# Optimization experiments

Hardware: AMD Instinct MI355X
Metric: run time of the kernel (lower is better)

The kernel has to match this reference:

```python
import jax, jax.numpy as jnp
import numpy as np

# Batched-graph geometry: 128 graphs x 400 nodes x 6400 edges
N_GRAPHS = 128
NODES_PER = 400
EDGES_PER = 6400
N_NODES = N_GRAPHS * NODES_PER      # 51200
N_EDGES = N_GRAPHS * EDGES_PER      # 819200
F_IN = 256
HID = 64
K = 8          # num_filtrations
D = 3          # outputs per coordinate function (4 funs -> 12 total)


def coord_feats(p, t_tri, t_gau, sig, W_lin, b_lin, c_rh, r_rh):
    """Apply the 4 coordinate transforms to persistence pairs p: [K, M, 2].
    Returns [M, K*4D] with layout cat-over-coordfuns inside, cat-over-filtrations outside,
    matching torch: cat([cat([mod(p_k) for mod in funs],1) for k],1)."""
    x0, x1 = p[..., 0:1], p[..., 1:2]                       # [K,M,1]
    tri = jax.nn.relu(x1 - jnp.abs(t_tri - x0))             # Triangle_transform -> [K,M,D]
    d2 = jnp.sum((p[..., None, :] - t_gau) ** 2, axis=-1)   # [K,M,D]
    gau = jnp.exp(-d2 / (2.0 * sig[0] ** 2))                # Gaussian_transform
    lin = p @ W_lin + b_lin                                 # Line_transform
    l1 = jnp.abs(x0 - c_rh) + jnp.abs(x1 - c_rh)            # L1 dist to centers
    rh = 1.0 / (1.0 + l1) - 1.0 / (1.0 + jnp.abs(jnp.abs(r_rh[0]) - l1))  # RationalHat
    feats = jnp.concatenate([tri, gau, lin, rh], axis=-1)   # [K,M,4D]
    Kk, M, Dd = feats.shape
    return feats.transpose(1, 0, 2).reshape(M, Kk * Dd)     # [M, K*4D]


def setup_inputs() -> dict:
    key = jax.random.key(0)
    ks = jax.random.split(key, 24)
    x = jax.random.normal(ks[0], (N_NODES, F_IN), jnp.float32)
    # edges drawn within each graph block
    offs = (jnp.arange(N_EDGES) // EDGES_PER) * NODES_PER
    edge_index = jax.random.randint(ks[1], (2, N_EDGES), 0, NODES_PER) + offs[None, :]
    batch_vec = jnp.arange(N_NODES) // NODES_PER            # graph id per node
    edge_slices = jnp.arange(N_GRAPHS + 1) * EDGES_PER
    s = lambda i, shape: (jax.random.normal(ks[i], shape, jnp.float32) * 0.1)
    inp = dict(
        x=x, edge_index=edge_index, batch_vec=batch_vec, edge_slices=edge_slices,
        # shared filtration MLP: Linear(F_IN,HID)-ReLU-Linear(HID,K)-ReLU
        W1=s(2, (F_IN, HID)), b1=jnp.zeros((HID,), jnp.float32),
        W2=s(3, (HID, K)), b2=jnp.zeros((K,), jnp.float32),
        # dim-0 coordinate-function params
        t_tri0=s(4, (D,)), t_gau0=s(5, (D, 2)), sig0=jnp.ones((1,), jnp.float32),
        W_lin0=s(6, (2, D)), b_lin0=jnp.zeros((D,), jnp.float32),
        c_rh0=s(7, (D,)), r_rh0=jnp.ones((1,), jnp.float32),
        # dim-1 coordinate-function params
        t_tri1=s(8, (D,)), t_gau1=s(9, (D, 2)), sig1=jnp.ones((1,), jnp.float32),
        W_lin1=s(10, (2, D)), b_lin1=jnp.zeros((D,), jnp.float32),
        c_rh1=s(11, (D,)), r_rh1=jnp.ones((1,), jnp.float32),
        # output linear: in = F_IN + 2*K*4D (dist_dim1=True, non-residual path)
        W_out=s(12, (F_IN + 2 * K * 4 * D, F_IN)), b_out=jnp.zeros((F_IN,), jnp.float32),
    )
    return inp


def reference(x, edge_index, batch_vec, edge_slices,
              W1, b1, W2, b2,
              t_tri0, t_gau0, sig0, W_lin0, b_lin0, c_rh0, r_rh0,
              t_tri1, t_gau1, sig1, W_lin1, b_lin1, c_rh1, r_rh1,
              W_out, b_out):
    # per-node filtration values (shared params, relu_filtrations)
    fv = jax.nn.relu(jax.nn.relu(x @ W1 + b1) @ W2 + b2)            # [N,K]
    # edge filtration = max of endpoint values
    fe = jnp.maximum(fv[edge_index[0]], fv[edge_index[1]])          # [E,K]
    # fake dim-0 persistence: pairs (v, v) for every vertex, per filtration
    pers0 = jnp.broadcast_to(fv.T[..., None], (K, fv.shape[0], 2))  # [K,N,2]
    # fake dim-1: one unpaired tuple per graph = max edge value, placed at first edge
    eb = batch_vec[edge_index[0]]                                   # [E] graph id per edge
    unpaired = jax.ops.segment_max(fe, eb, num_segments=N_GRAPHS)   # [B,K]
    chosen = edge_slices[:-1]                                       # deterministic edge per graph
    pers1 = jnp.zeros((edge_index.shape[1], K, 2), fv.dtype)
    pers1 = pers1.at[chosen, :, 0].set(unpaired)
    pers1 = pers1.transpose(1, 0, 2)                                # [K,E,2]
    # coordinate-function activations
    act0 = coord_feats(pers0, t_tri0, t_gau0, sig0, W_lin0, b_lin0, c_rh0, r_rh0)  # [N, K*12]
    mask = jnp.any(pers1 != 0, axis=(0, 2))                         # [E]
    act1 = coord_feats(pers1, t_tri1, t_gau1, sig1, W_lin1, b_lin1, c_rh1, r_rh1)  # [E, K*12]
    g1 = jax.ops.segment_sum(act1 * mask[:, None].astype(act1.dtype), eb,
                             num_segments=N_GRAPHS)                 # [B, K*12]
    concat = jnp.concatenate([x, act0, g1[batch_vec]], axis=1)      # [N, F_IN + 2*K*12]
    return jax.nn.relu(concat @ W_out + b_out)                      # [N, F_IN]
```

## Files before the change

kernel.cpp:

```cpp
#include <hip/hip_runtime.h>

#define N_GRAPHS 128
#define NODES_PER 400
#define EDGES_PER 6400
#define N_NODES (N_GRAPHS * NODES_PER)
#define N_EDGES (N_GRAPHS * EDGES_PER)
#define F_IN 256
#define HID 64
#define FEAT 96

typedef __attribute__((ext_vector_type(8))) short bf16x8;
typedef __attribute__((ext_vector_type(4))) float f32x4;

union u4b8 { uint4 u; bf16x8 v; };

__device__ __forceinline__ unsigned short f2b(float f) {
  union { float f; unsigned int u; } c; c.f = f;
  const unsigned int r = c.u + 0x7FFFu + ((c.u >> 16) & 1u);
  return (unsigned short)(r >> 16);
}

__device__ __forceinline__ void gload16(const void* g, void* l) {
  __builtin_amdgcn_global_load_lds(
      (const __attribute__((address_space(1))) unsigned int*)g,
      (__attribute__((address_space(3))) unsigned int*)l, 16, 0, 0);
}

__device__ __forceinline__ float coord_one(
    int fun, int d, float x0, float x1,
    const float* __restrict__ t_tri, const float* __restrict__ t_gau,
    const float* __restrict__ sig, const float* __restrict__ W_lin,
    const float* __restrict__ b_lin, const float* __restrict__ c_rh,
    const float* __restrict__ r_rh) {
  if (fun == 0) {
    return fmaxf(x1 - fabsf(t_tri[d] - x0), 0.f);
  } else if (fun == 1) {
    const float dx = x0 - t_gau[d * 2 + 0];
    const float dy = x1 - t_gau[d * 2 + 1];
    const float s = sig[0];
    return expf(-(dx * dx + dy * dy) / (2.f * s * s));
  } else if (fun == 2) {
    return x0 * W_lin[d] + x1 * W_lin[3 + d] + b_lin[d];
  } else {
    const float l1 = fabsf(x0 - c_rh[d]) + fabsf(x1 - c_rh[d]);
    return 1.f / (1.f + l1) - 1.f / (1.f + fabsf(fabsf(r_rh[0]) - l1));
  }
}

__global__ __launch_bounds__(256) void k_wt(
    const float* __restrict__ W_out, const float* __restrict__ W1,
    unsigned short* __restrict__ Wt2, unsigned short* __restrict__ Wt1c) {
  const int idx = blockIdx.x * 256 + threadIdx.x;
  if (idx < 384 * 256) {
    const int k = idx >> 8, c = idx & 255;
    const float v = (k < 352) ? W_out[(size_t)k * 256 + c] : 0.f;
    Wt2[((size_t)(k >> 3) * 256 + c) * 8 + (k & 7)] = f2b(v);
  } else {
    const int j = idx - 384 * 256;
    const int k = j >> 6, c = j & 63;
    Wt1c[((size_t)(k >> 3) * 64 + c) * 8 + (k & 7)] = f2b(W1[j]);
  }
}

__global__ __launch_bounds__(256, 3) void k_fv(
    const float* __restrict__ x, const unsigned short* __restrict__ Wt1c,
    const float* __restrict__ b1, const float* __restrict__ W2,
    const float* __restrict__ b2,
    const float* __restrict__ t_tri, const float* __restrict__ t_gau,
    const float* __restrict__ sig, const float* __restrict__ W_lin,
    const float* __restrict__ b_lin, const float* __restrict__ c_rh,
    const float* __restrict__ r_rh,
    float* __restrict__ fv, unsigned short* __restrict__ ext,
    unsigned short* __restrict__ xb, const int write_xb) {
  __shared__ float W2s[HID * 8];
  __shared__ float Hs[4][16][68];
  const int tid = threadIdx.x;
  const int wave = tid >> 6, lane = tid & 63;
  const int l15 = lane & 15, l4 = lane >> 4;
  const int n0 = blockIdx.x * 64;

  W2s[tid] = W2[tid];
  W2s[tid + 256] = W2[tid + 256];
  __syncthreads();

  const int arow = n0 + wave * 16 + l15;
  bf16x8 afr[8];
  #pragma unroll
  for (int kt = 0; kt < 8; ++kt) {
    const size_t go = (size_t)arow * F_IN + kt * 32 + l4 * 8;
    const float4 f0 = *(const float4*)&x[go];
    const float4 f1 = *(const float4*)&x[go + 4];
    u4b8 w;
    w.u.x = (unsigned)f2b(f0.x) | ((unsigned)f2b(f0.y) << 16);
    w.u.y = (unsigned)f2b(f0.z) | ((unsigned)f2b(f0.w) << 16);
    w.u.z = (unsigned)f2b(f1.x) | ((unsigned)f2b(f1.y) << 16);
    w.u.w = (unsigned)f2b(f1.z) | ((unsigned)f2b(f1.w) << 16);
    if (write_xb) *(uint4*)&xb[go] = w.u;
    afr[kt] = w.v;
  }

  f32x4 acc[4];
  #pragma unroll
  for (int nf = 0; nf < 4; ++nf) acc[nf] = (f32x4){0.f, 0.f, 0.f, 0.f};
  #pragma unroll
  for (int kt = 0; kt < 8; ++kt) {
    const unsigned short* wb = Wt1c + (size_t)(kt * 4 + l4) * 512;
    #pragma unroll
    for (int nf = 0; nf < 4; ++nf) {
      const bf16x8 b = *(const bf16x8*)&wb[(nf * 16 + l15) * 8];
      acc[nf] = __builtin_amdgcn_mfma_f32_16x16x32_bf16(afr[kt], b, acc[nf], 0, 0, 0);
    }
  }

  #pragma unroll
  for (int nf = 0; nf < 4; ++nf) {
    const int col = nf * 16 + l15;
    const float bb = b1[col];
    #pragma unroll
    for (int j = 0; j < 4; ++j)
      Hs[wave][l4 * 4 + j][col] = fmaxf(acc[nf][j] + bb, 0.f);
  }
  __syncthreads();

  #pragma unroll
  for (int p = tid; p < 512; p += 256) {
    const int row = p >> 3, kk = p & 7;
    const float* hr = Hs[row >> 4][row & 15];
    float s = b2[kk];
    #pragma unroll 8
    for (int j = 0; j < HID; ++j) s = fmaf(hr[j], W2s[j * 8 + kk], s);
    s = fmaxf(s, 0.f);
    const int n = n0 + row;
    fv[(size_t)n * 8 + kk] = s;

    unsigned short o[12] __attribute__((aligned(16)));
    #pragma unroll
    for (int fun = 0; fun < 4; ++fun)
      #pragma unroll
      for (int d = 0; d < 3; ++d)
        o[fun * 3 + d] = f2b(coord_one(fun, d, s, s,
                             t_tri, t_gau, sig, W_lin, b_lin, c_rh, r_rh));
    unsigned short* dst = &ext[(size_t)n * FEAT + kk * 12];
    *(uint2*)&dst[0] = *(const uint2*)&o[0];
    *(uint2*)&dst[4] = *(const uint2*)&o[4];
    *(uint2*)&dst[8] = *(const uint2*)&o[8];
  }
}

#define CHUNK (EDGES_PER / 8)
__global__ __launch_bounds__(256) void k_unpaired(
    const int* __restrict__ ei, const float* __restrict__ fv,
    float* __restrict__ unp) {
  __shared__ float lfv[NODES_PER * 8];
  __shared__ float red[256][8];
  const int g = blockIdx.x >> 3, ch = blockIdx.x & 7;
  const int tid = threadIdx.x;

  for (int i = tid; i < NODES_PER * 2; i += 256)
    *(float4*)&lfv[i * 4] = *(const float4*)&fv[(size_t)g * NODES_PER * 8 + i * 4];
  __syncthreads();

  float lm[8];
  #pragma unroll
  for (int k = 0; k < 8; ++k) lm[k] = 0.f;
  const int e0 = g * EDGES_PER + ch * CHUNK;
  for (int e = e0 + tid; e < e0 + CHUNK; e += 256) {
    const int a = ei[e] - g * NODES_PER;
    const int b = ei[N_EDGES + e] - g * NODES_PER;
    const float4 a0 = *(const float4*)&lfv[a * 8];
    const float4 a1 = *(const float4*)&lfv[a * 8 + 4];
    const float4 b0 = *(const float4*)&lfv[b * 8];
    const float4 b1 = *(const float4*)&lfv[b * 8 + 4];
    lm[0] = fmaxf(lm[0], fmaxf(a0.x, b0.x));
    lm[1] = fmaxf(lm[1], fmaxf(a0.y, b0.y));
    lm[2] = fmaxf(lm[2], fmaxf(a0.z, b0.z));
    lm[3] = fmaxf(lm[3], fmaxf(a0.w, b0.w));
    lm[4] = fmaxf(lm[4], fmaxf(a1.x, b1.x));
    lm[5] = fmaxf(lm[5], fmaxf(a1.y, b1.y));
    lm[6] = fmaxf(lm[6], fmaxf(a1.z, b1.z));
    lm[7] = fmaxf(lm[7], fmaxf(a1.w, b1.w));
  }
  #pragma unroll
  for (int k = 0; k < 8; ++k) red[tid][k] = lm[k];
  __syncthreads();
  for (int s = 128; s > 0; s >>= 1) {
    if (tid < s) {
      #pragma unroll
      for (int k = 0; k < 8; ++k)
        red[tid][k] = fmaxf(red[tid][k], red[tid + s][k]);
    }
    __syncthreads();
  }
  if (tid < 8)
    atomicMax((int*)&unp[g * 8 + tid], __float_as_int(red[0][tid]));
}

__global__ __launch_bounds__(256) void k_g1G(
    const float* __restrict__ unp, const float* __restrict__ t_tri,
    const float* __restrict__ t_gau, const float* __restrict__ sig,
    const float* __restrict__ W_lin, const float* __restrict__ b_lin,
    const float* __restrict__ c_rh, const float* __restrict__ r_rh,
    const float* __restrict__ W_out, const float* __restrict__ b_out,
    float* __restrict__ G) {
  const int g = blockIdx.x;
  const int t = threadIdx.x;
  __shared__ float u[8];
  __shared__ float feat[96];
  if (t < 8) u[t] = unp[g * 8 + t];
  __syncthreads();
  if (t < 96) {
    const float mask = (u[0] != 0.f || u[1] != 0.f || u[2] != 0.f ||
                        u[3] != 0.f || u[4] != 0.f || u[5] != 0.f ||
                        u[6] != 0.f || u[7] != 0.f) ? 1.f : 0.f;
    const int k = t / 12;
    const int fun = (t % 12) / 3;
    const int d = t % 3;
    feat[t] = mask * coord_one(fun, d, u[k], 0.f,
                               t_tri, t_gau, sig, W_lin, b_lin, c_rh, r_rh);
  }
  __syncthreads();
  float s = b_out[t];
  #pragma unroll 4
  for (int f = 0; f < 96; ++f)
    s = fmaf(feat[f], W_out[(size_t)(352 + f) * 256 + t], s);
  G[g * 256 + t] = s;
}

__global__ __launch_bounds__(256, 3) void k_out_mfma(
    const float* __restrict__ x, const unsigned short* __restrict__ xb,
    const unsigned short* __restrict__ ext, const unsigned short* __restrict__ zpad,
    const unsigned short* __restrict__ Wt2, const float* __restrict__ G,
    float* __restrict__ out, const int use_xb) {
  __shared__ unsigned short As[64 * 64];
  __shared__ unsigned short Bs[8][258][8];
  const int tid = threadIdx.x;
  const int wave = tid >> 6, lane = tid & 63;
  const int l15 = lane & 15, l4 = lane >> 4;
  const int n0 = blockIdx.x * 64;

  f32x4 acc[4][4];
  #pragma unroll
  for (int i = 0; i < 4; ++i)
    #pragma unroll
    for (int j = 0; j < 4; ++j)
      acc[i][j] = (f32x4){0.f, 0.f, 0.f, 0.f};

  for (int kt = 0; kt < 6; ++kt) {
    if (use_xb) {
      #pragma unroll
      for (int i = 0; i < 2; ++i) {
        const int jj = wave * 2 + i;
        const int r = jj * 8 + (lane >> 3);
        const int slot = lane & 7;
        const int c8 = slot ^ (r & 7);
        const int col = kt * 64 + c8 * 8;
        const int n = n0 + r;
        const unsigned short* src =
            (col < 256) ? &xb[(size_t)n * 256 + col]
          : (col < 352) ? &ext[(size_t)n * FEAT + (col - 256)]
                        : &zpad[slot * 8];
        gload16(src, &As[jj * 512]);
      }
    } else {
      #pragma unroll
      for (int rep = 0; rep < 2; ++rep) {
        const int u = tid + rep * 256;
        const int r = u >> 3, slot = u & 7;
        const int c8 = slot ^ (r & 7);
        const int col = kt * 64 + c8 * 8;
        const int n = n0 + r;
        uint4 w;
        if (col < 256) {
          const float4 f0 = *(const float4*)&x[(size_t)n * 256 + col];
          const float4 f1 = *(const float4*)&x[(size_t)n * 256 + col + 4];
          w.x = (unsigned)f2b(f0.x) | ((unsigned)f2b(f0.y) << 16);
          w.y = (unsigned)f2b(f0.z) | ((unsigned)f2b(f0.w) << 16);
          w.z = (unsigned)f2b(f1.x) | ((unsigned)f2b(f1.y) << 16);
          w.w = (unsigned)f2b(f1.z) | ((unsigned)f2b(f1.w) << 16);
        } else if (col < 352) {
          w = *(const uint4*)&ext[(size_t)n * FEAT + (col - 256)];
        } else {
          w = (uint4){0u, 0u, 0u, 0u};
        }
        *(uint4*)&As[u * 8] = w;
      }
    }
    #pragma unroll
    for (int i = 0; i < 8; ++i) {
      const int cB = wave * 8 + i;
      const int kcl = cB >> 2, cg = cB & 3;
      const unsigned short* src =
          &Wt2[((size_t)(kt * 8 + kcl) * 256 + cg * 64) * 8 + lane * 8];
      gload16(src, &Bs[kcl][cg * 64][0]);
    }
    __syncthreads();

    #pragma unroll
    for (int ks = 0; ks < 2; ++ks) {
      bf16x8 a[4], b[4];
      #pragma unroll
      for (int mf = 0; mf < 4; ++mf) {
        const int r = mf * 16 + l15;
        const int slot = (ks * 4 + l4) ^ (r & 7);
        a[mf] = *(const bf16x8*)&As[r * 64 + slot * 8];
      }
      #pragma unroll
      for (int nf = 0; nf < 4; ++nf)
        b[nf] = *(const bf16x8*)&Bs[ks * 4 + l4][wave * 64 + nf * 16 + l15][0];
      #pragma unroll
      for (int mf = 0; mf < 4; ++mf)
        #pragma unroll
        for (int nf = 0; nf < 4; ++nf)
          acc[mf][nf] = __builtin_amdgcn_mfma_f32_16x16x32_bf16(
              a[mf], b[nf], acc[mf][nf], 0, 0, 0);
    }
    __syncthreads();
  }

  #pragma unroll
  for (int mf = 0; mf < 4; ++mf) {
    const int rowb = n0 + mf * 16 + l4 * 4;
    #pragma unroll
    for (int j = 0; j < 4; ++j) {
      const int row = rowb + j;
      const float* Gr = &G[(row / NODES_PER) * 256];
      #pragma unroll
      for (int nf = 0; nf < 4; ++nf) {
        const int col = wave * 64 + nf * 16 + l15;
        out[(size_t)row * 256 + col] = fmaxf(acc[mf][nf][j] + Gr[col], 0.f);
      }
    }
  }
}

extern "C" void kernel_launch(void* const* d_in, const int* in_sizes, int n_in,
                              void* d_out, int out_size, void* d_ws, size_t ws_size,
                              hipStream_t stream) {
  const float* x          = (const float*)d_in[0];
  const int*   edge_index = (const int*)d_in[1];
  const float* W1     = (const float*)d_in[4];
  const float* b1     = (const float*)d_in[5];
  const float* W2     = (const float*)d_in[6];
  const float* b2     = (const float*)d_in[7];
  const float* t_tri0 = (const float*)d_in[8];
  const float* t_gau0 = (const float*)d_in[9];
  const float* sig0   = (const float*)d_in[10];
  const float* W_lin0 = (const float*)d_in[11];
  const float* b_lin0 = (const float*)d_in[12];
  const float* c_rh0  = (const float*)d_in[13];
  const float* r_rh0  = (const float*)d_in[14];
  const float* t_tri1 = (const float*)d_in[15];
  const float* t_gau1 = (const float*)d_in[16];
  const float* sig1   = (const float*)d_in[17];
  const float* W_lin1 = (const float*)d_in[18];
  const float* b_lin1 = (const float*)d_in[19];
  const float* c_rh1  = (const float*)d_in[20];
  const float* r_rh1  = (const float*)d_in[21];
  const float* W_out  = (const float*)d_in[22];
  const float* b_out  = (const float*)d_in[23];
  float* out = (float*)d_out;

  char* base = (char*)d_ws;
  float* fv            = (float*)(base + 0);
  float* unp           = (float*)(base + 1638400);
  float* G             = (float*)(base + 1642496);
  unsigned short* zpad = (unsigned short*)(base + 1773568);
  unsigned short* Wt2  = (unsigned short*)(base + 1773824);
  unsigned short* Wt1c = (unsigned short*)(base + 1970432);
  unsigned short* ext  = (unsigned short*)(base + 2003200);
  unsigned short* xb   = (unsigned short*)(base + 11833600);
  const size_t ws_need_xb = 11833600 + (size_t)N_NODES * F_IN * 2;
  const int use_xb = ws_size >= ws_need_xb ? 1 : 0;

  hipMemsetAsync(unp, 0, N_GRAPHS * 8 * sizeof(float), stream);
  hipMemsetAsync(zpad, 0, 256, stream);
  k_wt<<<(384 * 256 + F_IN * HID) / 256, 256, 0, stream>>>(W_out, W1, Wt2, Wt1c);
  k_fv<<<N_NODES / 64, 256, 0, stream>>>(
      x, Wt1c, b1, W2, b2,
      t_tri0, t_gau0, sig0, W_lin0, b_lin0, c_rh0, r_rh0,
      fv, ext, xb, use_xb);
  k_unpaired<<<N_GRAPHS * 8, 256, 0, stream>>>(edge_index, fv, unp);
  k_g1G<<<N_GRAPHS, 256, 0, stream>>>(unp, t_tri1, t_gau1, sig1,
                                      W_lin1, b_lin1, c_rh1, r_rh1,
                                      W_out, b_out, G);
  k_out_mfma<<<N_NODES / 64, 256, 0, stream>>>(x, xb, ext, zpad, Wt2, G,
                                               out, use_xb);
}
```

Baseline: 78.45 us.

## Double-buffer LDS tiles and use 8 waves per block in output GEMM

```diff
diff --git a/kernel.cpp b/kernel.cpp
--- a/kernel.cpp
+++ b/kernel.cpp
@@ -226,89 +226,102 @@
   G[g * 256 + t] = s;
 }
 
-__global__ __launch_bounds__(256, 3) void k_out_mfma(
+__global__ __launch_bounds__(512, 1) void k_out_mfma(
     const float* __restrict__ x, const unsigned short* __restrict__ xb,
     const unsigned short* __restrict__ ext, const unsigned short* __restrict__ zpad,
     const unsigned short* __restrict__ Wt2, const float* __restrict__ G,
     float* __restrict__ out, const int use_xb) {
-  __shared__ unsigned short As[64 * 64];
-  __shared__ unsigned short Bs[8][258][8];
+  __shared__ unsigned short As[2][64 * 64];
+  __shared__ unsigned short Bs[2][8][258][8];
   const int tid = threadIdx.x;
   const int wave = tid >> 6, lane = tid & 63;
+  const int wr = wave >> 2, wc = wave & 3;
   const int l15 = lane & 15, l4 = lane >> 4;
   const int n0 = blockIdx.x * 64;
 
-  f32x4 acc[4][4];
-  #pragma unroll
-  for (int i = 0; i < 4; ++i)
+  f32x4 acc[2][4];
+  #pragma unroll
+  for (int i = 0; i < 2; ++i)
     #pragma unroll
     for (int j = 0; j < 4; ++j)
       acc[i][j] = (f32x4){0.f, 0.f, 0.f, 0.f};
 
+  #define STAGE(KT, BUF)                                                     \
+    if (use_xb) {                                                            \
+      {                                                                      \
+        const int r = wave * 8 + (lane >> 3);                                \
+        const int slot = lane & 7;                                           \
+        const int c8 = slot ^ (r & 7);                                       \
+        const int col = (KT) * 64 + c8 * 8;                                  \
+        const int n = n0 + r;                                                \
+        const unsigned short* src =                                          \
+            (col < 256) ? &xb[(size_t)n * 256 + col]                         \
+          : (col < 352) ? &ext[(size_t)n * FEAT + (col - 256)]               \
+                        : &zpad[slot * 8];                                   \
+        gload16(src, &As[BUF][wave * 512]);                                  \
+      }                                                                      \
+      _Pragma("unroll")                                                      \
+      for (int i = 0; i < 4; ++i) {                                          \
+        const int cB = wave * 4 + i;                                         \
+        const int kcl = cB >> 2, cg = cB & 3;                                \
+        const unsigned short* src =                                          \
+            &Wt2[((size_t)((KT) * 8 + kcl) * 256 + cg * 64) * 8 + lane * 8]; \
+        gload16(src, &Bs[BUF][kcl][cg * 64][0]);                             \
+      }                                                                      \
+    } else {                                                                 \
+      {                                                                      \
+        const int r = tid >> 3, slot = tid & 7;                              \
+        const int c8 = slot ^ (r & 7);                                       \
+        const int col = (KT) * 64 + c8 * 8;                                  \
+        const int n = n0 + r;                                                \
+        uint4 w;                                                             \
+        if (col < 256) {                                                     \
+          const float4 f0 = *(const float4*)&x[(size_t)n * 256 + col];       \
+          const float4 f1 = *(const float4*)&x[(size_t)n * 256 + col + 4];   \
+          w.x = (unsigned)f2b(f0.x) | ((unsigned)f2b(f0.y) << 16);           \
+          w.y = (unsigned)f2b(f0.z) | ((unsigned)f2b(f0.w) << 16);           \
+          w.z = (unsigned)f2b(f1.x) | ((unsigned)f2b(f1.y) << 16);           \
+          w.w = (unsigned)f2b(f1.z) | ((unsigned)f2b(f1.w) << 16);           \
+        } else if (col < 352) {                                              \
+          w = *(const uint4*)&ext[(size_t)n * FEAT + (col - 256)];           \
+        } else {                                                             \
+          w = (uint4){0u, 0u, 0u, 0u};                                       \
+        }                                                                    \
+        *(uint4*)&As[BUF][tid * 8] = w;                                      \
+      }                                                                      \
+      _Pragma("unroll")                                                      \
+      for (int i = 0; i < 4; ++i) {                                          \
+        const int cB = wave * 4 + i;                                         \
+        const int kcl = cB >> 2, cg = cB & 3;                                \
+        *(uint4*)&Bs[BUF][kcl][cg * 64 + lane][0] =                          \
+            *(const uint4*)&Wt2[((size_t)((KT) * 8 + kcl) * 256 +            \
+                                 cg * 64) * 8 + lane * 8];                   \
+      }                                                                      \
+    }
+
+  STAGE(0, 0);
+  __syncthreads();
+
+  #pragma unroll
   for (int kt = 0; kt < 6; ++kt) {
-    if (use_xb) {
-      #pragma unroll
-      for (int i = 0; i < 2; ++i) {
-        const int jj = wave * 2 + i;
-        const int r = jj * 8 + (lane >> 3);
-        const int slot = lane & 7;
-        const int c8 = slot ^ (r & 7);
-        const int col = kt * 64 + c8 * 8;
-        const int n = n0 + r;
-        const unsigned short* src =
-            (col < 256) ? &xb[(size_t)n * 256 + col]
-          : (col < 352) ? &ext[(size_t)n * FEAT + (col - 256)]
-                        : &zpad[slot * 8];
-        gload16(src, &As[jj * 512]);
+    const int buf = kt & 1;
+    if (kt < 5) { STAGE(kt + 1, buf ^ 1); }
+
+    #pragma unroll
+    for (int ks = 0; ks < 2; ++ks) {
+      if (kt == 5 && ks == 1) continue;
+      bf16x8 a[2], b[4];
+      #pragma unroll
+      for (int mf = 0; mf < 2; ++mf) {
+        const int rl = wr * 32 + mf * 16 + l15;
+        const int slot = (ks * 4 + l4) ^ (rl & 7);
+        a[mf] = *(const bf16x8*)&As[buf][rl * 64 + slot * 8];
       }
-    } else {
-      #pragma unroll
-      for (int rep = 0; rep < 2; ++rep) {
-        const int u = tid + rep * 256;
-        const int r = u >> 3, slot = u & 7;
-        const int c8 = slot ^ (r & 7);
-        const int col = kt * 64 + c8 * 8;
-        const int n = n0 + r;
-        uint4 w;
-        if (col < 256) {
-          const float4 f0 = *(const float4*)&x[(size_t)n * 256 + col];
-          const float4 f1 = *(const float4*)&x[(size_t)n * 256 + col + 4];
-          w.x = (unsigned)f2b(f0.x) | ((unsigned)f2b(f0.y) << 16);
-          w.y = (unsigned)f2b(f0.z) | ((unsigned)f2b(f0.w) << 16);
-          w.z = (unsigned)f2b(f1.x) | ((unsigned)f2b(f1.y) << 16);
-          w.w = (unsigned)f2b(f1.z) | ((unsigned)f2b(f1.w) << 16);
-        } else if (col < 352) {
-          w = *(const uint4*)&ext[(size_t)n * FEAT + (col - 256)];
-        } else {
-          w = (uint4){0u, 0u, 0u, 0u};
-        }
-        *(uint4*)&As[u * 8] = w;
-      }
-    }
-    #pragma unroll
-    for (int i = 0; i < 8; ++i) {
-      const int cB = wave * 8 + i;
-      const int kcl = cB >> 2, cg = cB & 3;
-      const unsigned short* src =
-          &Wt2[((size_t)(kt * 8 + kcl) * 256 + cg * 64) * 8 + lane * 8];
-      gload16(src, &Bs[kcl][cg * 64][0]);
-    }
-    __syncthreads();
-
-    #pragma unroll
-    for (int ks = 0; ks < 2; ++ks) {
-      bf16x8 a[4], b[4];
-      #pragma unroll
-      for (int mf = 0; mf < 4; ++mf) {
-        const int r = mf * 16 + l15;
-        const int slot = (ks * 4 + l4) ^ (r & 7);
-        a[mf] = *(const bf16x8*)&As[r * 64 + slot * 8];
-      }
       #pragma unroll
       for (int nf = 0; nf < 4; ++nf)
-        b[nf] = *(const bf16x8*)&Bs[ks * 4 + l4][wave * 64 + nf * 16 + l15][0];
-      #pragma unroll
-      for (int mf = 0; mf < 4; ++mf)
+        b[nf] = *(const bf16x8*)&Bs[buf][ks * 4 + l4][wc * 64 + nf * 16 + l15][0];
+      #pragma unroll
+      for (int mf = 0; mf < 2; ++mf)
         #pragma unroll
         for (int nf = 0; nf < 4; ++nf)
           acc[mf][nf] = __builtin_amdgcn_mfma_f32_16x16x32_bf16(
@@ -316,17 +329,18 @@
     }
     __syncthreads();
   }
-
-  #pragma unroll
-  for (int mf = 0; mf < 4; ++mf) {
-    const int rowb = n0 + mf * 16 + l4 * 4;
+  #undef STAGE
+
+  #pragma unroll
+  for (int mf = 0; mf < 2; ++mf) {
+    const int rowb = n0 + wr * 32 + mf * 16 + l4 * 4;
     #pragma unroll
     for (int j = 0; j < 4; ++j) {
       const int row = rowb + j;
       const float* Gr = &G[(row / NODES_PER) * 256];
       #pragma unroll
       for (int nf = 0; nf < 4; ++nf) {
-        const int col = wave * 64 + nf * 16 + l15;
+        const int col = wc * 64 + nf * 16 + l15;
         out[(size_t)row * 256 + col] = fmaxf(acc[mf][nf][j] + Gr[col], 0.f);
       }
     }
@@ -383,6 +397,6 @@
   k_g1G<<<N_GRAPHS, 256, 0, stream>>>(unp, t_tri1, t_gau1, sig1,
                                       W_lin1, b_lin1, c_rh1, r_rh1,
                                       W_out, b_out, G);
-  k_out_mfma<<<N_NODES / 64, 256, 0, stream>>>(x, xb, ext, zpad, Wt2, G,
+  k_out_mfma<<<N_NODES / 64, 512, 0, stream>>>(x, xb, ext, zpad, Wt2, G,
                                                out, use_xb);
 }
```

Measured after the change: 86.52 us. 10.3% more time.
